# Kernel optimization log

Measured on AMD Instinct MI355X. Metric: run time of the kernel, lower is better.

The kernel has to match this reference:

```python
import jax, jax.numpy as jnp
import numpy as np

N = 50000   # nodes
E = 800000  # edges (avg degree 16)
D = 256     # input = hidden = output dim
L = 3       # num_layers


def setup_inputs() -> dict:
    key = jax.random.key(0)
    k0, k1, k2, k3 = jax.random.split(key, 4)
    x = jax.random.normal(k0, (N, D), dtype=jnp.float32)
    edge_index = jax.random.randint(k1, (2, E), 0, N, dtype=jnp.int32)
    # SAGEConv params per layer: lin_l (neighbor path, with bias), lin_r (root path)
    Wl = jax.random.normal(k2, (L, D, D), dtype=jnp.float32) * 0.05
    Wr = jax.random.normal(k3, (L, D, D), dtype=jnp.float32) * 0.05
    b = jnp.zeros((L, D), dtype=jnp.float32)
    return {"x": x, "edge_index": edge_index, "Wl": Wl, "Wr": Wr, "b": b}


def reference(x, edge_index, Wl, Wr, b):
    src = edge_index[0]
    dst = edge_index[1]
    # in-degree for mean aggregation (clamped to avoid div-by-zero)
    deg = jax.ops.segment_sum(jnp.ones((E,), x.dtype), dst, num_segments=N)
    inv_deg = (1.0 / jnp.maximum(deg, 1.0))[:, None]  # [N,1]
    h = x
    for i in range(L):
        # gather source features, scatter-add into destinations, then mean
        agg = jax.ops.segment_sum(h[src], dst, num_segments=N) * inv_deg  # [N,D]
        h = agg @ Wl[i] + h @ Wr[i] + b[i]
        if i < L - 1:
            h = jax.nn.relu(h)  # dropout(p=0.1) is identity in eval mode
    return h
```

## Files before the change

kernel.cpp:

```cpp
#include <hip/hip_runtime.h>


typedef __attribute__((ext_vector_type(8))) _Float16 f16x8;
typedef __attribute__((ext_vector_type(4))) float f32x4;

__global__ void count_deg_kernel(const int* __restrict__ dst,
                                 int* __restrict__ deg, int E) {
    int i = (blockIdx.x * blockDim.x + threadIdx.x) * 2;
    if (i + 1 < E) {
        int2 d = *(const int2*)&dst[i];
        atomicAdd(&deg[d.x], 1);
        atomicAdd(&deg[d.y], 1);
    } else if (i < E) {
        atomicAdd(&deg[dst[i]], 1);
    }
}

__device__ __forceinline__ int block_excl_scan_256(int v, int tid) {
    int lane = tid & 63, w = tid >> 6;
    int x = v;
#pragma unroll
    for (int off = 1; off < 64; off <<= 1) {
        int y = __shfl_up(x, off);
        if (lane >= off) x += y;
    }
    __shared__ int wsum[4], woff[4];
    if (lane == 63) wsum[w] = x;
    __syncthreads();
    if (tid == 0) {
        int a = 0;
#pragma unroll
        for (int i = 0; i < 4; ++i) { woff[i] = a; a += wsum[i]; }
    }
    __syncthreads();
    return woff[w] + x - v;
}

__global__ void scan_phase1(const int* __restrict__ deg,
                            int* __restrict__ partial, int n) {
    int base = blockIdx.x * 1024;
    int s = 0;
    for (int i = threadIdx.x; i < 1024; i += 256) {
        int idx = base + i;
        s += (idx < n) ? deg[idx] : 0;
    }
    __shared__ int ws4[4];
    int lane = threadIdx.x & 63, w = threadIdx.x >> 6;
#pragma unroll
    for (int off = 32; off; off >>= 1) s += __shfl_down(s, off);
    if (lane == 0) ws4[w] = s;
    __syncthreads();
    if (threadIdx.x == 0)
        partial[blockIdx.x] = ws4[0] + ws4[1] + ws4[2] + ws4[3];
}

__global__ void scan_phase2(int* __restrict__ partial, int nb,
                            int* __restrict__ rowptr, int n, int E) {
    int tid = threadIdx.x;
    int v = (tid < nb) ? partial[tid] : 0;
    int ex = block_excl_scan_256(v, tid);
    if (tid < nb) partial[tid] = ex;
    if (tid == 0) rowptr[n] = E;
}

__global__ void scan_phase3(const int* __restrict__ deg,
                            const int* __restrict__ partial,
                            int* __restrict__ rowptr, int* __restrict__ cursor,
                            float* __restrict__ inv_deg, int n) {
    int base = blockIdx.x * 1024 + threadIdx.x * 4;
    int d[4];
#pragma unroll
    for (int j = 0; j < 4; ++j) {
        int idx = base + j;
        d[j] = (idx < n) ? deg[idx] : 0;
    }
    int tsum = d[0] + d[1] + d[2] + d[3];
    int ex = block_excl_scan_256(tsum, threadIdx.x);
    int run = partial[blockIdx.x] + ex;
#pragma unroll
    for (int j = 0; j < 4; ++j) {
        int idx = base + j;
        if (idx < n) {
            rowptr[idx] = run;
            cursor[idx] = run;
            inv_deg[idx] = 1.0f / (float)max(d[j], 1);
        }
        run += d[j];
    }
}

__global__ void fill_csr_kernel(const int* __restrict__ src,
                                const int* __restrict__ dst,
                                int* __restrict__ cursor,
                                int* __restrict__ csr_src, int E) {
    int i = (blockIdx.x * blockDim.x + threadIdx.x) * 2;
    if (i + 1 < E) {
        int2 d = *(const int2*)&dst[i];
        int2 s = *(const int2*)&src[i];
        int p0 = atomicAdd(&cursor[d.x], 1);
        csr_src[p0] = s.x;
        int p1 = atomicAdd(&cursor[d.y], 1);
        csr_src[p1] = s.y;
    } else if (i < E) {
        int p = atomicAdd(&cursor[dst[i]], 1);
        csr_src[p] = src[i];
    }
}

__global__ void presplit_w_kernel(const float* __restrict__ Wl,
                                  const float* __restrict__ Wr,
                                  _Float16* __restrict__ Wf,
                                  int* __restrict__ deg, int N, int total) {
    int idx = blockIdx.x * blockDim.x + threadIdx.x;
    if (idx < N) deg[idx] = 0;
    if (idx >= total) return;
    int l = idx >> 17;
    int rem = idx & 131071;
    int s = rem >> 16;
    int kc = rem & 65535;
    int k = kc >> 8, c = kc & 255;
    const float* W = s ? Wr : Wl;
    float w = W[((size_t)l * 256 + k) * 256 + c];
    int k0c = k >> 5, g = (k >> 3) & 3, j = k & 7;
    int tile = c >> 4, col = c & 15;
    int fi = (l * 2 + s) * 65536 + k0c * 8192 + ((tile * 4 + g) * 16 + col) * 8 + j;
    Wf[fi] = (_Float16)w;
}

__device__ __forceinline__ void gemm_from_lds64(
    const _Float16 (*Ah)[65][8], int tid, const _Float16* __restrict__ Wf_l,
    const float* __restrict__ bias, _Float16* __restrict__ zl,
    _Float16* __restrict__ zr, int r0, int M) {
    const int wave = tid >> 6, lane = tid & 63;
    const int l15 = lane & 15, lg = lane >> 4;
    const int wr = (wave & 1) * 32;
    const int wc = (wave >> 1) * 64;
    const int tg0 = wc >> 4;
    const _Float16* wbase = Wf_l + (lg * 16 + l15) * 8;

    f32x4 accl[2][4], accr[2][4];
#pragma unroll
    for (int rt = 0; rt < 2; ++rt)
#pragma unroll
        for (int t = 0; t < 4; ++t) {
            accl[rt][t] = (f32x4)(0.0f);
            accr[rt][t] = (f32x4)(0.0f);
        }

    f16x8 blc[4], brc[4];
#pragma unroll
    for (int t = 0; t < 4; ++t) {
        blc[t] = *(const f16x8*)&wbase[(tg0 + t) * 512];
        brc[t] = *(const f16x8*)&wbase[65536 + (tg0 + t) * 512];
    }

#pragma unroll
    for (int s = 0; s < 8; ++s) {
        f16x8 bln[4], brn[4];
        if (s < 7) {
            const _Float16* wn = wbase + (s + 1) * 8192;
#pragma unroll
            for (int t = 0; t < 4; ++t) {
                bln[t] = *(const f16x8*)&wn[(tg0 + t) * 512];
                brn[t] = *(const f16x8*)&wn[65536 + (tg0 + t) * 512];
            }
        }
        f16x8 a0 = *(const f16x8*)&Ah[s * 4 + lg][wr + l15][0];
        f16x8 a1 = *(const f16x8*)&Ah[s * 4 + lg][wr + 16 + l15][0];
#pragma unroll
        for (int t = 0; t < 4; ++t) {
            accl[0][t] = __builtin_amdgcn_mfma_f32_16x16x32_f16(a0, blc[t],
                                                                accl[0][t], 0, 0, 0);
            accl[1][t] = __builtin_amdgcn_mfma_f32_16x16x32_f16(a1, blc[t],
                                                                accl[1][t], 0, 0, 0);
            accr[0][t] = __builtin_amdgcn_mfma_f32_16x16x32_f16(a0, brc[t],
                                                                accr[0][t], 0, 0, 0);
            accr[1][t] = __builtin_amdgcn_mfma_f32_16x16x32_f16(a1, brc[t],
                                                                accr[1][t], 0, 0, 0);
        }
        if (s < 7) {
#pragma unroll
            for (int t = 0; t < 4; ++t) {
                blc[t] = bln[t];
                brc[t] = brn[t];
            }
        }
    }

    float bv[4];
#pragma unroll
    for (int t = 0; t < 4; ++t) bv[t] = bias[wc + t * 16 + l15];
#pragma unroll
    for (int rt = 0; rt < 2; ++rt) {
#pragma unroll
        for (int r = 0; r < 4; ++r) {
            int grow = r0 + wr + rt * 16 + lg * 4 + r;
            if (grow >= M) continue;
#pragma unroll
            for (int t = 0; t < 4; ++t) {
                int col = wc + t * 16 + l15;
                zl[(size_t)grow * 256 + col] = (_Float16)accl[rt][t][r];
                zr[(size_t)grow * 256 + col] =
                    (_Float16)(accr[rt][t][r] + bv[t]);
            }
        }
    }
}

__global__ __launch_bounds__(512) void gemm0_kernel(
    const float* __restrict__ xsrc, _Float16* __restrict__ zl,
    _Float16* __restrict__ zr, const _Float16* __restrict__ Wf_l,
    const float* __restrict__ bias, int M) {
    __shared__ __align__(16) _Float16 Ah[32][65][8];
    const int tid = threadIdx.x;
    const int r0 = blockIdx.x * 64;
#pragma unroll
    for (int i = 0; i < 4; ++i) {
        int idx = i * 512 + tid;
        int row = idx >> 5, g = idx & 31;
        int grow = r0 + row;
        f16x8 v = (f16x8)(_Float16)0;
        if (grow < M) {
            const float4* p = (const float4*)&xsrc[(size_t)grow * 256 + g * 8];
            float4 v0 = p[0], v1 = p[1];
            v[0] = (_Float16)v0.x; v[1] = (_Float16)v0.y;
            v[2] = (_Float16)v0.z; v[3] = (_Float16)v0.w;
            v[4] = (_Float16)v1.x; v[5] = (_Float16)v1.y;
            v[6] = (_Float16)v1.z; v[7] = (_Float16)v1.w;
        }
        *(f16x8*)&Ah[g][row][0] = v;
    }
    __syncthreads();
    gemm_from_lds64(Ah, tid, Wf_l, bias, zl, zr, r0, M);
}

__global__ __launch_bounds__(512) void fused_layer_kernel(
    const _Float16* __restrict__ zl_in, const _Float16* __restrict__ zr_in,
    _Float16* __restrict__ zl_out, _Float16* __restrict__ zr_out,
    const int* __restrict__ rowptr, const int* __restrict__ csr_src,
    const float* __restrict__ inv_deg, const _Float16* __restrict__ Wf_l,
    const float* __restrict__ bias, int M) {
    __shared__ __align__(16) _Float16 Ah[32][65][8];
    const int tid = threadIdx.x;
    const int hw = tid >> 5, li = tid & 31;
    const int r0 = blockIdx.x * 64;

#pragma unroll
    for (int i = 0; i < 4; ++i) {
        int row = hw * 4 + i;
        int v = r0 + row;
        f16x8 hv = (f16x8)(_Float16)0;
        if (v < M) {
            int beg = rowptr[v], end = rowptr[v + 1];
            float sc = inv_deg[v];
            f16x8 zp = *(const f16x8*)&zr_in[(size_t)v * 256 + li * 8];
            float acc[8] = {0.f, 0.f, 0.f, 0.f, 0.f, 0.f, 0.f, 0.f};
            for (int e = beg; e < end; e += 8) {
                f16x8 t[8];
#pragma unroll
                for (int k = 0; k < 8; ++k) {
                    int ee = min(e + k, end - 1);
                    int u = csr_src[ee];
                    t[k] = *(const f16x8*)&zl_in[(size_t)u * 256 + li * 8];
                }
#pragma unroll
                for (int k = 0; k < 8; ++k) {
                    if (e + k < end) {
#pragma unroll
                        for (int j = 0; j < 8; ++j) acc[j] += (float)t[k][j];
                    }
                }
            }
#pragma unroll
            for (int j = 0; j < 8; ++j)
                hv[j] = (_Float16)fmaxf(acc[j] * sc + (float)zp[j], 0.0f);
        }
        *(f16x8*)&Ah[li][row][0] = hv;
    }
    __syncthreads();
    gemm_from_lds64(Ah, tid, Wf_l, bias, zl_out, zr_out, r0, M);
}

__global__ void combine_final_kernel(const _Float16* __restrict__ zl,
                                     const _Float16* __restrict__ zr,
                                     const int* __restrict__ rowptr,
                                     const int* __restrict__ csr_src,
                                     const float* __restrict__ inv_deg,
                                     float* __restrict__ fout, int n) {
    int hw = threadIdx.x >> 5, li = threadIdx.x & 31;
    int v = blockIdx.x * 8 + hw;
    if (v >= n) return;
    int beg = rowptr[v], end = rowptr[v + 1];
    float acc[8] = {0.f, 0.f, 0.f, 0.f, 0.f, 0.f, 0.f, 0.f};
    for (int e = beg; e < end; e += 8) {
        f16x8 t[8];
#pragma unroll
        for (int k = 0; k < 8; ++k) {
            int ee = min(e + k, end - 1);
            int u = csr_src[ee];
            t[k] = *(const f16x8*)&zl[(size_t)u * 256 + li * 8];
        }
#pragma unroll
        for (int k = 0; k < 8; ++k) {
            if (e + k < end) {
#pragma unroll
                for (int j = 0; j < 8; ++j) acc[j] += (float)t[k][j];
            }
        }
    }
    float sc = inv_deg[v];
    f16x8 zp = *(const f16x8*)&zr[(size_t)v * 256 + li * 8];
    float o[8];
#pragma unroll
    for (int j = 0; j < 8; ++j) o[j] = acc[j] * sc + (float)zp[j];
    float4* op = (float4*)&fout[(size_t)v * 256 + li * 8];
    op[0] = make_float4(o[0], o[1], o[2], o[3]);
    op[1] = make_float4(o[4], o[5], o[6], o[7]);
}

extern "C" void kernel_launch(void* const* d_in, const int* in_sizes, int n_in,
                              void* d_out, int out_size, void* d_ws, size_t ws_size,
                              hipStream_t stream) {
    const int D = 256;
    const int N = in_sizes[0] / D;
    const int E = in_sizes[1] / 2;
    const int L = in_sizes[2] / (D * D);

    const float* x  = (const float*)d_in[0];
    const int*   ei = (const int*)d_in[1];
    const float* Wl = (const float*)d_in[2];
    const float* Wr = (const float*)d_in[3];
    const float* b  = (const float*)d_in[4];
    const int* src = ei;
    const int* dst = ei + E;

    size_t off = 0;
    auto alloc = [&](size_t bytes) {
        void* p = (char*)d_ws + off;
        off += (bytes + 255) & ~(size_t)255;
        return p;
    };
    int*   deg     = (int*)alloc((size_t)N * 4);
    int*   rowptr  = (int*)alloc((size_t)(N + 1) * 4);
    int*   cursor  = (int*)alloc((size_t)N * 4);
    float* inv_deg = (float*)alloc((size_t)N * 4);
    int*   csr_src = (int*)alloc((size_t)E * 4);
    int*   partial = (int*)alloc(256 * 4);
    _Float16* zlA = (_Float16*)alloc((size_t)N * D * 2);
    _Float16* zrA = (_Float16*)alloc((size_t)N * D * 2);
    _Float16* Wf  = (_Float16*)alloc((size_t)L * 2 * 65536 * 2);
    (void)ws_size;

    _Float16* zlB = (_Float16*)d_out;
    _Float16* zrB = zlB + (size_t)N * D;
    float* outf = (float*)d_out;

    const int scan_blocks = (N + 1023) / 1024;

    int wtotal = L * 2 * 65536;
    hipLaunchKernelGGL(presplit_w_kernel, dim3((wtotal + 255) / 256), dim3(256),
                       0, stream, Wl, Wr, Wf, deg, N, wtotal);

    hipLaunchKernelGGL(count_deg_kernel, dim3((E / 2 + 255) / 256), dim3(256),
                       0, stream, dst, deg, E);
    hipLaunchKernelGGL(scan_phase1, dim3(scan_blocks), dim3(256), 0, stream,
                       deg, partial, N);
    hipLaunchKernelGGL(scan_phase2, dim3(1), dim3(256), 0, stream,
                       partial, scan_blocks, rowptr, N, E);
    hipLaunchKernelGGL(scan_phase3, dim3(scan_blocks), dim3(256), 0, stream,
                       deg, partial, rowptr, cursor, inv_deg, N);
    hipLaunchKernelGGL(fill_csr_kernel, dim3((E / 2 + 255) / 256), dim3(256),
                       0, stream, src, dst, cursor, csr_src, E);

    const int gemm_blocks = (N + 63) / 64;
    const int comb_blocks = (N + 7) / 8;

    hipLaunchKernelGGL(gemm0_kernel, dim3(gemm_blocks), dim3(512), 0, stream,
                       x, zlA, zrA, Wf, b, N);
    hipLaunchKernelGGL(fused_layer_kernel, dim3(gemm_blocks), dim3(512), 0,
                       stream, zlA, zrA, zlB, zrB, rowptr, csr_src, inv_deg,
                       Wf + 131072, b + D, N);
    hipLaunchKernelGGL(fused_layer_kernel, dim3(gemm_blocks), dim3(512), 0,
                       stream, zlB, zrB, zlA, zrA, rowptr, csr_src, inv_deg,
                       Wf + 262144, b + 2 * D, N);
    hipLaunchKernelGGL(combine_final_kernel, dim3(comb_blocks), dim3(256), 0,
                       stream, zlA, zrA, rowptr, csr_src, inv_deg, outf, N);
}
```

Measured before the change: 370.6 us.

## Unfuse gather from GEMM and slice feature columns across blocks for cache locality

Splits the fused aggregate+GEMM layer kernel into a standalone GEMM kernel and a column-sliced gather/combine kernel that writes an fp16 hidden buffer. Each combine block handles one 32-column slice for 256 nodes, so concurrent blocks gather narrower rows of zl. The aim is a smaller random-gather working set with better L2 hit rates and higher occupancy than the 512-thread fused kernel. In exchange it adds an extra write and read of an N×256 fp16 intermediate per layer, two more kernel launches, and 8x more per-node edge-index reads.

```diff
diff --git a/kernel.cpp b/kernel.cpp
--- a/kernel.cpp
+++ b/kernel.cpp
@@ -207,10 +207,10 @@
     }
 }
 
-__global__ __launch_bounds__(512) void gemm0_kernel(
-    const float* __restrict__ xsrc, _Float16* __restrict__ zl,
-    _Float16* __restrict__ zr, const _Float16* __restrict__ Wf_l,
-    const float* __restrict__ bias, int M) {
+__global__ __launch_bounds__(512) void gemm_dual_kernel(
+    const float* __restrict__ xsrc, const _Float16* __restrict__ hsrc,
+    int f32src, _Float16* __restrict__ zl, _Float16* __restrict__ zr,
+    const _Float16* __restrict__ Wf_l, const float* __restrict__ bias, int M) {
     __shared__ __align__(16) _Float16 Ah[32][65][8];
     const int tid = threadIdx.x;
     const int r0 = blockIdx.x * 64;
@@ -221,12 +221,17 @@
         int grow = r0 + row;
         f16x8 v = (f16x8)(_Float16)0;
         if (grow < M) {
-            const float4* p = (const float4*)&xsrc[(size_t)grow * 256 + g * 8];
-            float4 v0 = p[0], v1 = p[1];
-            v[0] = (_Float16)v0.x; v[1] = (_Float16)v0.y;
-            v[2] = (_Float16)v0.z; v[3] = (_Float16)v0.w;
-            v[4] = (_Float16)v1.x; v[5] = (_Float16)v1.y;
-            v[6] = (_Float16)v1.z; v[7] = (_Float16)v1.w;
+            if (f32src) {
+                const float4* p =
+                    (const float4*)&xsrc[(size_t)grow * 256 + g * 8];
+                float4 v0 = p[0], v1 = p[1];
+                v[0] = (_Float16)v0.x; v[1] = (_Float16)v0.y;
+                v[2] = (_Float16)v0.z; v[3] = (_Float16)v0.w;
+                v[4] = (_Float16)v1.x; v[5] = (_Float16)v1.y;
+                v[6] = (_Float16)v1.z; v[7] = (_Float16)v1.w;
+            } else {
+                v = *(const f16x8*)&hsrc[(size_t)grow * 256 + g * 8];
+            }
         }
         *(f16x8*)&Ah[g][row][0] = v;
     }
@@ -234,88 +239,55 @@
     gemm_from_lds64(Ah, tid, Wf_l, bias, zl, zr, r0, M);
 }
 
-__global__ __launch_bounds__(512) void fused_layer_kernel(
-    const _Float16* __restrict__ zl_in, const _Float16* __restrict__ zr_in,
-    _Float16* __restrict__ zl_out, _Float16* __restrict__ zr_out,
+__global__ __launch_bounds__(256) void combine_sliced_kernel(
+    const _Float16* __restrict__ zl, const _Float16* __restrict__ zr,
     const int* __restrict__ rowptr, const int* __restrict__ csr_src,
-    const float* __restrict__ inv_deg, const _Float16* __restrict__ Wf_l,
-    const float* __restrict__ bias, int M) {
-    __shared__ __align__(16) _Float16 Ah[32][65][8];
-    const int tid = threadIdx.x;
-    const int hw = tid >> 5, li = tid & 31;
-    const int r0 = blockIdx.x * 64;
+    const float* __restrict__ inv_deg, _Float16* __restrict__ hout,
+    float* __restrict__ fout, int n, int mode) {
+    const int slice = blockIdx.x & 7;
+    const int chunk = blockIdx.x >> 3;
+    const int grp = threadIdx.x >> 2;
+    const int l4 = threadIdx.x & 3;
+    const int cbase = slice * 32 + l4 * 8;
 
 #pragma unroll
     for (int i = 0; i < 4; ++i) {
-        int row = hw * 4 + i;
-        int v = r0 + row;
-        f16x8 hv = (f16x8)(_Float16)0;
-        if (v < M) {
-            int beg = rowptr[v], end = rowptr[v + 1];
-            float sc = inv_deg[v];
-            f16x8 zp = *(const f16x8*)&zr_in[(size_t)v * 256 + li * 8];
-            float acc[8] = {0.f, 0.f, 0.f, 0.f, 0.f, 0.f, 0.f, 0.f};
-            for (int e = beg; e < end; e += 8) {
-                f16x8 t[8];
-#pragma unroll
-                for (int k = 0; k < 8; ++k) {
-                    int ee = min(e + k, end - 1);
-                    int u = csr_src[ee];
-                    t[k] = *(const f16x8*)&zl_in[(size_t)u * 256 + li * 8];
+        int v = chunk * 256 + i * 64 + grp;
+        if (v >= n) continue;
+        int beg = rowptr[v], end = rowptr[v + 1];
+        float acc[8] = {0.f, 0.f, 0.f, 0.f, 0.f, 0.f, 0.f, 0.f};
+        for (int e = beg; e < end; e += 8) {
+            f16x8 t[8];
+#pragma unroll
+            for (int k = 0; k < 8; ++k) {
+                int ee = min(e + k, end - 1);
+                int u = csr_src[ee];
+                t[k] = *(const f16x8*)&zl[(size_t)u * 256 + cbase];
+            }
+#pragma unroll
+            for (int k = 0; k < 8; ++k) {
+                if (e + k < end) {
+#pragma unroll
+                    for (int j = 0; j < 8; ++j) acc[j] += (float)t[k][j];
                 }
-#pragma unroll
-                for (int k = 0; k < 8; ++k) {
-                    if (e + k < end) {
-#pragma unroll
-                        for (int j = 0; j < 8; ++j) acc[j] += (float)t[k][j];
-                    }
-                }
-            }
-#pragma unroll
-            for (int j = 0; j < 8; ++j)
-                hv[j] = (_Float16)fmaxf(acc[j] * sc + (float)zp[j], 0.0f);
-        }
-        *(f16x8*)&Ah[li][row][0] = hv;
-    }
-    __syncthreads();
-    gemm_from_lds64(Ah, tid, Wf_l, bias, zl_out, zr_out, r0, M);
-}
-
-__global__ void combine_final_kernel(const _Float16* __restrict__ zl,
-                                     const _Float16* __restrict__ zr,
-                                     const int* __restrict__ rowptr,
-                                     const int* __restrict__ csr_src,
-                                     const float* __restrict__ inv_deg,
-                                     float* __restrict__ fout, int n) {
-    int hw = threadIdx.x >> 5, li = threadIdx.x & 31;
-    int v = blockIdx.x * 8 + hw;
-    if (v >= n) return;
-    int beg = rowptr[v], end = rowptr[v + 1];
-    float acc[8] = {0.f, 0.f, 0.f, 0.f, 0.f, 0.f, 0.f, 0.f};
-    for (int e = beg; e < end; e += 8) {
-        f16x8 t[8];
-#pragma unroll
-        for (int k = 0; k < 8; ++k) {
-            int ee = min(e + k, end - 1);
-            int u = csr_src[ee];
-            t[k] = *(const f16x8*)&zl[(size_t)u * 256 + li * 8];
-        }
-#pragma unroll
-        for (int k = 0; k < 8; ++k) {
-            if (e + k < end) {
-#pragma unroll
-                for (int j = 0; j < 8; ++j) acc[j] += (float)t[k][j];
-            }
-        }
-    }
-    float sc = inv_deg[v];
-    f16x8 zp = *(const f16x8*)&zr[(size_t)v * 256 + li * 8];
-    float o[8];
-#pragma unroll
-    for (int j = 0; j < 8; ++j) o[j] = acc[j] * sc + (float)zp[j];
-    float4* op = (float4*)&fout[(size_t)v * 256 + li * 8];
-    op[0] = make_float4(o[0], o[1], o[2], o[3]);
-    op[1] = make_float4(o[4], o[5], o[6], o[7]);
+            }
+        }
+        float sc = inv_deg[v];
+        f16x8 zp = *(const f16x8*)&zr[(size_t)v * 256 + cbase];
+        float o[8];
+#pragma unroll
+        for (int j = 0; j < 8; ++j) o[j] = acc[j] * sc + (float)zp[j];
+        if (mode == 0) {
+            f16x8 hv;
+#pragma unroll
+            for (int j = 0; j < 8; ++j) hv[j] = (_Float16)fmaxf(o[j], 0.0f);
+            *(f16x8*)&hout[(size_t)v * 256 + cbase] = hv;
+        } else {
+            float4* op = (float4*)&fout[(size_t)v * 256 + cbase];
+            op[0] = make_float4(o[0], o[1], o[2], o[3]);
+            op[1] = make_float4(o[4], o[5], o[6], o[7]);
+        }
+    }
 }
 
 extern "C" void kernel_launch(void* const* d_in, const int* in_sizes, int n_in,
@@ -348,6 +320,7 @@
     int*   partial = (int*)alloc(256 * 4);
     _Float16* zlA = (_Float16*)alloc((size_t)N * D * 2);
     _Float16* zrA = (_Float16*)alloc((size_t)N * D * 2);
+    _Float16* hbuf = (_Float16*)alloc((size_t)N * D * 2);
     _Float16* Wf  = (_Float16*)alloc((size_t)L * 2 * 65536 * 2);
     (void)ws_size;
 
@@ -373,16 +346,24 @@
                        0, stream, src, dst, cursor, csr_src, E);
 
     const int gemm_blocks = (N + 63) / 64;
-    const int comb_blocks = (N + 7) / 8;
-
-    hipLaunchKernelGGL(gemm0_kernel, dim3(gemm_blocks), dim3(512), 0, stream,
-                       x, zlA, zrA, Wf, b, N);
-    hipLaunchKernelGGL(fused_layer_kernel, dim3(gemm_blocks), dim3(512), 0,
-                       stream, zlA, zrA, zlB, zrB, rowptr, csr_src, inv_deg,
+    const int comb_blocks = 8 * ((N + 255) / 256);
+
+    hipLaunchKernelGGL(gemm_dual_kernel, dim3(gemm_blocks), dim3(512), 0,
+                       stream, x, (const _Float16*)nullptr, 1, zlA, zrA,
+                       Wf, b, N);
+    hipLaunchKernelGGL(combine_sliced_kernel, dim3(comb_blocks), dim3(256), 0,
+                       stream, zlA, zrA, rowptr, csr_src, inv_deg,
+                       hbuf, outf, N, 0);
+    hipLaunchKernelGGL(gemm_dual_kernel, dim3(gemm_blocks), dim3(512), 0,
+                       stream, (const float*)nullptr, hbuf, 0, zlB, zrB,
                        Wf + 131072, b + D, N);
-    hipLaunchKernelGGL(fused_layer_kernel, dim3(gemm_blocks), dim3(512), 0,
-                       stream, zlB, zrB, zlA, zrA, rowptr, csr_src, inv_deg,
+    hipLaunchKernelGGL(combine_sliced_kernel, dim3(comb_blocks), dim3(256), 0,
+                       stream, zlB, zrB, rowptr, csr_src, inv_deg,
+                       hbuf, outf, N, 0);
+    hipLaunchKernelGGL(gemm_dual_kernel, dim3(gemm_blocks), dim3(512), 0,
+                       stream, (const float*)nullptr, hbuf, 0, zlA, zrA,
                        Wf + 262144, b + 2 * D, N);
-    hipLaunchKernelGGL(combine_final_kernel, dim3(comb_blocks), dim3(256), 0,
-                       stream, zlA, zrA, rowptr, csr_src, inv_deg, outf, N);
-}
+    hipLaunchKernelGGL(combine_sliced_kernel, dim3(comb_blocks), dim3(256), 0,
+                       stream, zlA, zrA, rowptr, csr_src, inv_deg,
+                       hbuf, outf, N, 1);
+}
```

Measured after the change: 513.2 us. +38.5%, slower.
